# Kernel tuning notes

Measured on AMD Instinct MI355X. Metric: run time of the kernel, lower is better.

## Reference

```python
import jax, jax.numpy as jnp
import numpy as np

B, N, NPOINT, NSAMPLE = 8, 8192, 2048, 64
RADIUS = 0.2
C_IN = 64  # input feature channels; mlp[0]=64 -> 67 after use_xyz concat


def setup_inputs() -> dict:
    key = jax.random.key(0)
    ks = jax.random.split(key, 12)
    xyz = jax.random.uniform(ks[0], (B, N, 3), dtype=jnp.float32)
    features = jax.random.normal(ks[1], (B, N, C_IN), dtype=jnp.float32)
    inds = jax.random.randint(ks[2], (B, NPOINT), 0, N, dtype=jnp.int32)

    def mkw(k, cin, cout):
        return jax.random.normal(k, (cin, cout), jnp.float32) * (1.0 / np.sqrt(cin).astype(np.float32))

    w0 = mkw(ks[3], C_IN + 3, 64)
    w1 = mkw(ks[4], 64, 64)
    w2 = mkw(ks[5], 64, 128)
    # BN (inference) folded into per-channel scale/shift
    s0 = 1.0 + 0.1 * jax.random.normal(ks[6], (64,), jnp.float32)
    t0 = 0.1 * jax.random.normal(ks[7], (64,), jnp.float32)
    s1 = 1.0 + 0.1 * jax.random.normal(ks[8], (64,), jnp.float32)
    t1 = 0.1 * jax.random.normal(ks[9], (64,), jnp.float32)
    s2 = 1.0 + 0.1 * jax.random.normal(ks[10], (128,), jnp.float32)
    t2 = 0.1 * jax.random.normal(ks[11], (128,), jnp.float32)
    return dict(xyz=xyz, features=features, inds=inds,
                w0=w0, s0=s0, t0=t0, w1=w1, s1=s1, t1=t1, w2=w2, s2=s2, t2=t2)


def _ball_query(xyz, new_xyz):
    """First NSAMPLE point indices within RADIUS of each query; pad by repeating
    the first hit (matches CUDA ball_query semantics). xyz:(B,N,3) new_xyz:(B,S,3)."""
    nn = jnp.sum(xyz * xyz, axis=-1)            # (B,N)
    qq = jnp.sum(new_xyz * new_xyz, axis=-1)    # (B,S)
    d2 = qq[:, :, None] + nn[:, None, :] - 2.0 * jnp.einsum('bsc,bnc->bsn', new_xyz, xyz)
    within = d2 < (RADIUS * RADIUS)
    ar = jnp.arange(N, dtype=jnp.int32)
    keyed = jnp.where(within, ar[None, None, :], N)   # out-of-radius -> sentinel N
    keyed = jnp.sort(keyed, axis=-1)[:, :, :NSAMPLE]  # first hits in point order
    idx = jnp.where(keyed == N, keyed[:, :, :1], keyed)
    return jnp.minimum(idx, N - 1)


_gather = jax.vmap(lambda pts, i: pts[i])  # (N,C),(M,) -> (M,C) per batch


def reference(xyz, features, inds, w0, s0, t0, w1, s1, t1, w2, s2, t2):
    new_xyz = _gather(xyz, inds)                              # (B,S,3)
    idx = _ball_query(xyz, new_xyz)                           # (B,S,ns)
    flat = idx.reshape(B, NPOINT * NSAMPLE)
    g_xyz = _gather(xyz, flat).reshape(B, NPOINT, NSAMPLE, 3)
    g_xyz = (g_xyz - new_xyz[:, :, None, :]) / RADIUS         # normalize_xyz
    g_feat = _gather(features, flat).reshape(B, NPOINT, NSAMPLE, C_IN)
    x = jnp.concatenate([g_xyz, g_feat], axis=-1)             # (B,S,ns,C+3)
    for wgt, s, t in ((w0, s0, t0), (w1, s1, t1), (w2, s2, t2)):
        x = jax.nn.relu(jnp.einsum('bpsc,cd->bpsd', x, wgt) * s + t)
    new_features = jnp.max(x, axis=2)                         # max-pool over nsample
    return new_xyz, new_features, inds, idx
```

## Files before the change

### kernel.cpp

```cpp
#include <hip/hip_runtime.h>

#define BB 8
#define NN 8192
#define NPOINT 2048
#define NSAMPLE 64
#define CIN 64
#define RADIUS 0.2f
#define R2 (RADIUS * RADIUS)

#define OFF_NEWXYZ 0
#define OFF_FEAT (BB * NPOINT * 3)
#define OFF_INDS (OFF_FEAT + BB * NPOINT * 128)
#define OFF_IDX (OFF_INDS + BB * NPOINT)

typedef _Float16 half8 __attribute__((ext_vector_type(8)));
typedef _Float16 half4 __attribute__((ext_vector_type(4)));
typedef __fp16 f16x2 __attribute__((ext_vector_type(2)));
typedef float floatx16 __attribute__((ext_vector_type(16)));

#define P0 88
#define P1 72
#define X_LOC 0
#define H_LOC (64 * P0)
#define XH_WAVE (64 * P0 + 64 * P1)
#define WT0_S 0
#define WT1_S (64 * P0)
#define WT2_S (64 * P0 + 64 * P1)

#define QPW 8

__global__ __launch_bounds__(256) void ballq_kernel(
    const float* __restrict__ xyz, const int* __restrict__ inds,
    float* __restrict__ out, const float* __restrict__ features,
    _Float16* __restrict__ f16f) {
  if (f16f) {
    const int t = blockIdx.x * 256 + threadIdx.x;
    const float4* src = (const float4*)features;
    const float4 a = src[2 * t + 0];
    const float4 b = src[2 * t + 1];
    union {
      half8 v;
      f16x2 p[4];
    } u;
    u.p[0] = __builtin_amdgcn_cvt_pkrtz(a.x, a.y);
    u.p[1] = __builtin_amdgcn_cvt_pkrtz(a.z, a.w);
    u.p[2] = __builtin_amdgcn_cvt_pkrtz(b.x, b.y);
    u.p[3] = __builtin_amdgcn_cvt_pkrtz(b.z, b.w);
    ((half8*)f16f)[t] = u.v;
  }

  __shared__ int sidx[4][2][NSAMPLE];
  const int wave = (blockIdx.x * 256 + threadIdx.x) >> 6;
  const int lane = threadIdx.x & 63;
  const int wid = threadIdx.x >> 6;
  const int q0 = wave * 2, q1 = q0 + 1;
  const int b = q0 >> 11;

  const float* xb = xyz + (size_t)b * NN * 3;
  const int i0 = inds[q0], i1 = inds[q1];
  const float c0x = xb[i0 * 3 + 0], c0y = xb[i0 * 3 + 1], c0z = xb[i0 * 3 + 2];
  const float c1x = xb[i1 * 3 + 0], c1y = xb[i1 * 3 + 1], c1z = xb[i1 * 3 + 2];

  if (lane < 2) {
    const int qq_ = lane ? q1 : q0;
    const int ii = lane ? i1 : i0;
    out[OFF_NEWXYZ + (size_t)qq_ * 3 + 0] = lane ? c1x : c0x;
    out[OFF_NEWXYZ + (size_t)qq_ * 3 + 1] = lane ? c1y : c0y;
    out[OFF_NEWXYZ + (size_t)qq_ * 3 + 2] = lane ? c1z : c0z;
    out[OFF_INDS + qq_] = (float)ii;
  }

  const float qq0 = c0x * c0x + c0y * c0y + c0z * c0z;
  const float qq1 = c1x * c1x + c1y * c1y + c1z * c1z;

  int cnt0 = 0, cnt1 = 0;
  float ax[4], ay[4], az[4];
#pragma unroll
  for (int k = 0; k < 4; ++k) {
    const float* p = xb + (size_t)(k * 64 + lane) * 3;
    ax[k] = p[0];
    ay[k] = p[1];
    az[k] = p[2];
  }
  for (int j0 = 0; j0 < NN; j0 += 256) {
    float bx[4] = {0}, by[4] = {0}, bz[4] = {0};
    const int jn = j0 + 256;
    if (jn < NN) {
#pragma unroll
      for (int k = 0; k < 4; ++k) {
        const float* p = xb + (size_t)(jn + k * 64 + lane) * 3;
        bx[k] = p[0];
        by[k] = p[1];
        bz[k] = p[2];
      }
    }
#pragma unroll
    for (int k = 0; k < 4; ++k) {
      const int j = j0 + k * 64 + lane;
      const float nn_ = ax[k] * ax[k] + ay[k] * ay[k] + az[k] * az[k];
      const float dot0 = c0x * ax[k] + c0y * ay[k] + c0z * az[k];
      const float dot1 = c1x * ax[k] + c1y * ay[k] + c1z * az[k];
      const bool hit0 = (qq0 + nn_ - 2.0f * dot0) < R2;
      const bool hit1 = (qq1 + nn_ - 2.0f * dot1) < R2;
      const unsigned long long m0 = __ballot(hit0);
      const unsigned long long m1 = __ballot(hit1);
      if (hit0) {
        const int pos = cnt0 + (int)__popcll(m0 & ((1ull << lane) - 1ull));
        if (pos < NSAMPLE) sidx[wid][0][pos] = j;
      }
      if (hit1) {
        const int pos = cnt1 + (int)__popcll(m1 & ((1ull << lane) - 1ull));
        if (pos < NSAMPLE) sidx[wid][1][pos] = j;
      }
      cnt0 += (int)__popcll(m0);
      cnt1 += (int)__popcll(m1);
    }
    if (cnt0 >= NSAMPLE && cnt1 >= NSAMPLE) break;
#pragma unroll
    for (int k = 0; k < 4; ++k) {
      ax[k] = bx[k];
      ay[k] = by[k];
      az[k] = bz[k];
    }
  }
  const int v0 = sidx[wid][0][lane < cnt0 ? lane : 0];
  out[OFF_IDX + (size_t)q0 * NSAMPLE + lane] = (float)v0;
  const int v1 = sidx[wid][1][lane < cnt1 ? lane : 0];
  out[OFF_IDX + (size_t)q1 * NSAMPLE + lane] = (float)v1;
}

template <bool F16>
__global__ __launch_bounds__(128, 2) void mlp_mfma(
    const float* __restrict__ xyz, const float* __restrict__ features,
    const _Float16* __restrict__ f16f, const int* __restrict__ inds,
    const float* __restrict__ w0, const float* __restrict__ s0,
    const float* __restrict__ t0, const float* __restrict__ w1,
    const float* __restrict__ s1, const float* __restrict__ t1,
    const float* __restrict__ w2, const float* __restrict__ s2,
    const float* __restrict__ t2, float* __restrict__ out) {
  __shared__ _Float16 sm[2 * XH_WAVE];
  const int tid = threadIdx.x;
  const int w = tid >> 6;
  const int l = tid & 63;
  const int l31 = l & 31;
  const int h5 = l >> 5;
  const int koff = h5 * 8;

  {
    const int d = tid >> 1, hf = tid & 1;
    const float sd0 = s0[d], td0 = t0[d], sd1 = s1[d];
#pragma unroll
    for (int j = 0; j < 44; ++j) {
      const int c = hf * 44 + j;
      float v = 0.0f;
      if (c < 64) v = w0[(3 + c) * 64 + d] * sd0;
      else if (c < 67) v = w0[(c - 64) * 64 + d] * sd0;
      else if (c == 67) v = td0;
      sm[WT0_S + d * P0 + c] = (_Float16)v;
    }
#pragma unroll
    for (int j = 0; j < 32; ++j) {
      const int c = hf * 32 + j;
      sm[WT1_S + d * P1 + c] = (_Float16)(w1[c * 64 + d] * sd1);
    }
    const int ch = tid;
    const float sch = s2[ch];
#pragma unroll
    for (int c = 0; c < 64; ++c)
      sm[WT2_S + ch * P1 + c] = (_Float16)(w2[c * 128 + ch] * sch);
  }
  __syncthreads();

  half8 b0f[2][5], b1f[2][4], b2f[4][4];
#pragma unroll
  for (int nt = 0; nt < 2; ++nt)
#pragma unroll
    for (int ks = 0; ks < 5; ++ks)
      b0f[nt][ks] =
          *(const half8*)&sm[WT0_S + (nt * 32 + l31) * P0 + ks * 16 + koff];
#pragma unroll
  for (int nt = 0; nt < 2; ++nt)
#pragma unroll
    for (int ks = 0; ks < 4; ++ks)
      b1f[nt][ks] =
          *(const half8*)&sm[WT1_S + (nt * 32 + l31) * P1 + ks * 16 + koff];
#pragma unroll
  for (int ct = 0; ct < 4; ++ct)
#pragma unroll
    for (int ks = 0; ks < 4; ++ks)
      b2f[ct][ks] =
          *(const half8*)&sm[WT2_S + (ct * 32 + l31) * P1 + ks * 16 + koff];
  const float t1v0 = t1[l31];
  const float t1v1 = t1[32 + l31];
  float t2v[4];
#pragma unroll
  for (int ct = 0; ct < 4; ++ct) t2v[ct] = t2[ct * 32 + l31];
  __syncthreads();

  _Float16* xbuf = sm + w * XH_WAVE + X_LOC;
  _Float16* hbuf = sm + w * XH_WAVE + H_LOC;
  {
    half8 z = {};
    *(half8*)&xbuf[l * P0 + 72] = z;
  }

  const int lb = (blockIdx.x & 7) * ((int)gridDim.x >> 3) + (blockIdx.x >> 3);
  const int wq0 = (lb * 2 + w) * QPW;
  const int b = wq0 >> 11;
  const float* xb = xyz + (size_t)b * NN * 3;
  const float* fbase = features + (size_t)b * NN * CIN;
  const _Float16* fb16 = f16f + (size_t)b * NN * CIN;

  int myidx = (int)out[OFF_IDX + (size_t)wq0 * NSAMPLE + l];
  int indv = inds[wq0];
  float cx = xb[indv * 3 + 0], cy = xb[indv * 3 + 1], cz = xb[indv * 3 + 2];
  float ppx = xb[myidx * 3 + 0], ppy = xb[myidx * 3 + 1],
        ppz = xb[myidx * 3 + 2];

#pragma unroll 1
  for (int qi = 0; qi < QPW; ++qi) {
    const int q = wq0 + qi;
    const int nq = (qi + 1 < QPW) ? q + 1 : q;

    float4 g[16];
    half8 gh[8];
    if constexpr (F16) {
#pragma unroll
      for (int i = 0; i < 8; ++i) {
        const int r = (l >> 3) + 8 * i;
        const int sidx = __shfl(myidx, r, 64);
        gh[i] = *(const half8*)(fb16 + (size_t)sidx * CIN + (l & 7) * 8);
      }
    } else {
#pragma unroll
      for (int i = 0; i < 16; ++i) {
        const int s = (l >> 2) + 16 * (i & 3);
        const int c = (l & 3) + 4 * (i >> 2);
        const int sidx = __shfl(myidx, s, 64);
        g[i] = *(const float4*)(fbase + (size_t)sidx * CIN + 4 * c);
      }
    }
    const float fni = out[OFF_IDX + (size_t)nq * NSAMPLE + l];
    const int nindv = inds[nq];

    if constexpr (F16) {
#pragma unroll
      for (int i = 0; i < 8; ++i) {
        const int r = (l >> 3) + 8 * i;
        *(half8*)&xbuf[r * P0 + (l & 7) * 8] = gh[i];
      }
    } else {
#pragma unroll
      for (int i = 0; i < 16; ++i) {
        const int s = (l >> 2) + 16 * (i & 3);
        const int c = (l & 3) + 4 * (i >> 2);
        union {
          half4 v;
          f16x2 p[2];
        } hv;
        hv.p[0] = __builtin_amdgcn_cvt_pkrtz(g[i].x, g[i].y);
        hv.p[1] = __builtin_amdgcn_cvt_pkrtz(g[i].z, g[i].w);
        *(half4*)&xbuf[s * P0 + 4 * c] = hv.v;
      }
    }
    {
      union {
        half8 v;
        f16x2 p[4];
      } xv;
      xv.p[0] =
          __builtin_amdgcn_cvt_pkrtz((ppx - cx) * 5.0f, (ppy - cy) * 5.0f);
      xv.p[1] = __builtin_amdgcn_cvt_pkrtz((ppz - cz) * 5.0f, 1.0f);
      xv.p[2] = __builtin_amdgcn_cvt_pkrtz(0.0f, 0.0f);
      xv.p[3] = __builtin_amdgcn_cvt_pkrtz(0.0f, 0.0f);
      *(half8*)&xbuf[l * P0 + 64] = xv.v;
    }

    {
      half8 xa[2][5];
#pragma unroll
      for (int st = 0; st < 2; ++st)
#pragma unroll
        for (int ks = 0; ks < 5; ++ks)
          xa[st][ks] =
              *(const half8*)&xbuf[(st * 32 + l31) * P0 + ks * 16 + koff];
#pragma unroll
      for (int nt = 0; nt < 2; ++nt)
#pragma unroll
        for (int st = 0; st < 2; ++st) {
          floatx16 acc;
#pragma unroll
          for (int i = 0; i < 16; ++i) acc[i] = 0.0f;
#pragma unroll
          for (int ks = 0; ks < 5; ++ks)
            acc = __builtin_amdgcn_mfma_f32_32x32x16_f16(xa[st][ks],
                                                         b0f[nt][ks], acc,
                                                         0, 0, 0);
#pragma unroll
          for (int reg = 0; reg < 16; ++reg) {
            const int row = st * 32 + (reg & 3) + 8 * (reg >> 2) + 4 * h5;
            hbuf[row * P1 + nt * 32 + l31] = (_Float16)fmaxf(acc[reg], 0.0f);
          }
        }
    }

    const int nidxs = (int)fni;
    const float ncx = xb[nindv * 3 + 0];
    const float ncy = xb[nindv * 3 + 1];
    const float ncz = xb[nindv * 3 + 2];
    const float nppx = xb[nidxs * 3 + 0];
    const float nppy = xb[nidxs * 3 + 1];
    const float nppz = xb[nidxs * 3 + 2];

    {
      half8 ha[2][4];
#pragma unroll
      for (int st = 0; st < 2; ++st)
#pragma unroll
        for (int ks = 0; ks < 4; ++ks)
          ha[st][ks] =
              *(const half8*)&hbuf[(st * 32 + l31) * P1 + ks * 16 + koff];
#pragma unroll
      for (int nt = 0; nt < 2; ++nt) {
        const float tt = nt ? t1v1 : t1v0;
#pragma unroll
        for (int st = 0; st < 2; ++st) {
          floatx16 acc;
#pragma unroll
          for (int i = 0; i < 16; ++i) acc[i] = 0.0f;
#pragma unroll
          for (int ks = 0; ks < 4; ++ks)
            acc = __builtin_amdgcn_mfma_f32_32x32x16_f16(ha[st][ks],
                                                         b1f[nt][ks], acc,
                                                         0, 0, 0);
#pragma unroll
          for (int reg = 0; reg < 16; ++reg) {
            const int row = st * 32 + (reg & 3) + 8 * (reg >> 2) + 4 * h5;
            xbuf[row * P0 + nt * 32 + l31] =
                (_Float16)fmaxf(acc[reg] + tt, 0.0f);
          }
        }
      }
    }

    {
      half8 h1a[2][4];
#pragma unroll
      for (int st = 0; st < 2; ++st)
#pragma unroll
        for (int ks = 0; ks < 4; ++ks)
          h1a[st][ks] =
              *(const half8*)&xbuf[(st * 32 + l31) * P0 + ks * 16 + koff];
#pragma unroll
      for (int ct = 0; ct < 4; ++ct) {
        floatx16 aA, aB;
#pragma unroll
        for (int i = 0; i < 16; ++i) {
          aA[i] = 0.0f;
          aB[i] = 0.0f;
        }
#pragma unroll
        for (int ks = 0; ks < 4; ++ks) {
          aA = __builtin_amdgcn_mfma_f32_32x32x16_f16(h1a[0][ks], b2f[ct][ks],
                                                      aA, 0, 0, 0);
          aB = __builtin_amdgcn_mfma_f32_32x32x16_f16(h1a[1][ks], b2f[ct][ks],
                                                      aB, 0, 0, 0);
        }
        float m = fmaxf(aA[0], aB[0]);
#pragma unroll
        for (int i = 1; i < 16; ++i) m = fmaxf(m, fmaxf(aA[i], aB[i]));
        float v = fmaxf(m + t2v[ct], 0.0f);
        v = fmaxf(v, __shfl_xor(v, 32, 64));
        if (l < 32) out[OFF_FEAT + (size_t)q * 128 + ct * 32 + l] = v;
      }
    }

    myidx = nidxs;
    cx = ncx; cy = ncy; cz = ncz;
    ppx = nppx; ppy = nppy; ppz = nppz;
  }
}

extern "C" void kernel_launch(void* const* d_in, const int* in_sizes, int n_in,
                              void* d_out, int out_size, void* d_ws,
                              size_t ws_size, hipStream_t stream) {
  const float* xyz = (const float*)d_in[0];
  const float* features = (const float*)d_in[1];
  const int* inds = (const int*)d_in[2];
  const float* w0 = (const float*)d_in[3];
  const float* s0 = (const float*)d_in[4];
  const float* t0 = (const float*)d_in[5];
  const float* w1 = (const float*)d_in[6];
  const float* s1 = (const float*)d_in[7];
  const float* t1 = (const float*)d_in[8];
  const float* w2 = (const float*)d_in[9];
  const float* s2 = (const float*)d_in[10];
  const float* t2 = (const float*)d_in[11];
  float* out = (float*)d_out;

  const size_t f16need = (size_t)BB * NN * CIN * sizeof(_Float16);
  _Float16* f16f = (ws_size >= f16need) ? (_Float16*)d_ws : nullptr;

  const int nquery = BB * NPOINT;
  ballq_kernel<<<nquery / 8, 256, 0, stream>>>(xyz, inds, out, features, f16f);
  if (f16f)
    mlp_mfma<true><<<nquery / (2 * QPW), 128, 0, stream>>>(
        xyz, features, f16f, inds, w0, s0, t0, w1, s1, t1, w2, s2, t2, out);
  else
    mlp_mfma<false><<<nquery / (2 * QPW), 128, 0, stream>>>(
        xyz, features, f16f, inds, w0, s0, t0, w1, s1, t1, w2, s2, t2, out);
}
```

Baseline: 175.5 us.

## Prefold MLP weights to fp16 in workspace and stream them from global

The first kernel now also writes fp16 copies of the three MLP weight matrices, with BN scale folded in, into the workspace. A new MLP kernel loads the weight fragments directly from global/L2 every query instead of staging them in shared memory. This cuts LDS per block so three blocks fit per CU, and halves queries per wave, doubling the grid. The trade-off is repeated global weight reads per query, extra register pressure, and a serial weight-prep step done by block 0.

```diff
diff --git a/kernel.cpp b/kernel.cpp
--- a/kernel.cpp
+++ b/kernel.cpp
@@ -27,13 +27,24 @@
 #define WT1_S (64 * P0)
 #define WT2_S (64 * P0 + 64 * P1)
 
-#define QPW 8
+#define QPW_FB 8
+#define QPW_G 4
+
+#define WSF16H (BB * NN * CIN)
+#define WT0_OFF WSF16H
+#define WT1_OFF (WT0_OFF + 64 * 80)
+#define WT2_OFF (WT1_OFF + 64 * 64)
+#define WS_END (WT2_OFF + 128 * 64)
+#define WS_NEED ((size_t)WS_END * 2)
 
 __global__ __launch_bounds__(256) void ballq_kernel(
     const float* __restrict__ xyz, const int* __restrict__ inds,
     float* __restrict__ out, const float* __restrict__ features,
-    _Float16* __restrict__ f16f) {
-  if (f16f) {
+    _Float16* __restrict__ ws16, const float* __restrict__ w0,
+    const float* __restrict__ s0, const float* __restrict__ t0,
+    const float* __restrict__ w1, const float* __restrict__ s1,
+    const float* __restrict__ w2, const float* __restrict__ s2) {
+  if (ws16) {
     const int t = blockIdx.x * 256 + threadIdx.x;
     const float4* src = (const float4*)features;
     const float4 a = src[2 * t + 0];
@@ -46,7 +57,32 @@
     u.p[1] = __builtin_amdgcn_cvt_pkrtz(a.z, a.w);
     u.p[2] = __builtin_amdgcn_cvt_pkrtz(b.x, b.y);
     u.p[3] = __builtin_amdgcn_cvt_pkrtz(b.z, b.w);
-    ((half8*)f16f)[t] = u.v;
+    ((half8*)ws16)[t] = u.v;
+    if (blockIdx.x == 0) {
+      const int tt = threadIdx.x;
+      if (tt < 64) {
+        const int d = tt;
+        const float sd = s0[d], td = t0[d];
+        _Float16* row = ws16 + WT0_OFF + d * 80;
+        for (int c = 0; c < 80; ++c) {
+          float v = 0.0f;
+          if (c < 64) v = w0[(3 + c) * 64 + d] * sd;
+          else if (c < 67) v = w0[(c - 64) * 64 + d] * sd;
+          else if (c == 67) v = td;
+          row[c] = (_Float16)v;
+        }
+      } else if (tt < 128) {
+        const int d = tt - 64;
+        const float sd = s1[d];
+        _Float16* row = ws16 + WT1_OFF + d * 64;
+        for (int c = 0; c < 64; ++c) row[c] = (_Float16)(w1[c * 64 + d] * sd);
+      } else {
+        const int d2 = tt - 128;
+        const float sd = s2[d2];
+        _Float16* row = ws16 + WT2_OFF + d2 * 64;
+        for (int c = 0; c < 64; ++c) row[c] = (_Float16)(w2[c * 128 + d2] * sd);
+      }
+    }
   }
 
   __shared__ int sidx[4][2][NSAMPLE];
@@ -129,10 +165,215 @@
   out[OFF_IDX + (size_t)q1 * NSAMPLE + lane] = (float)v1;
 }
 
-template <bool F16>
-__global__ __launch_bounds__(128, 2) void mlp_mfma(
+__global__ __launch_bounds__(128, 3) void mlp_g(
+    const float* __restrict__ xyz, const _Float16* __restrict__ ws16,
+    const int* __restrict__ inds, const float* __restrict__ t1,
+    const float* __restrict__ t2, float* __restrict__ out) {
+  __shared__ _Float16 sm[2 * 64 * P0];
+  const int tid = threadIdx.x;
+  const int w = tid >> 6;
+  const int l = tid & 63;
+  const int l31 = l & 31;
+  const int h5 = l >> 5;
+  const int koff = h5 * 8;
+
+  _Float16* xbuf = sm + w * (64 * P0);
+  {
+    half8 z = {};
+    *(half8*)&xbuf[l * P0 + 72] = z;
+  }
+
+  const int lb = (blockIdx.x & 7) * ((int)gridDim.x >> 3) + (blockIdx.x >> 3);
+  const int wq0 = (lb * 2 + w) * QPW_G;
+  const int b = wq0 >> 11;
+  const float* xb = xyz + (size_t)b * NN * 3;
+  const _Float16* fb16 = ws16 + (size_t)b * NN * CIN;
+
+  const float t1v0 = t1[l31];
+  const float t1v1 = t1[32 + l31];
+  float t2v[4];
+#pragma unroll
+  for (int ct = 0; ct < 4; ++ct) t2v[ct] = t2[ct * 32 + l31];
+
+  int myidx = (int)out[OFF_IDX + (size_t)wq0 * NSAMPLE + l];
+  int indv = inds[wq0];
+  float cx = xb[indv * 3 + 0], cy = xb[indv * 3 + 1], cz = xb[indv * 3 + 2];
+  float ppx = xb[myidx * 3 + 0], ppy = xb[myidx * 3 + 1],
+        ppz = xb[myidx * 3 + 2];
+
+  unsigned long long wbu = (unsigned long long)(ws16 + WT0_OFF);
+
+#pragma unroll 1
+  for (int qi = 0; qi < QPW_G; ++qi) {
+    const int q = wq0 + qi;
+    const int nq = (qi + 1 < QPW_G) ? q + 1 : q;
+    asm volatile("" : "+s"(wbu));
+    const _Float16* wt0 = (const _Float16*)wbu;
+    const _Float16* wt1q = wt0 + 64 * 80;
+    const _Float16* wt2q = wt0 + 64 * 80 + 64 * 64;
+
+    half8 gh[8];
+#pragma unroll
+    for (int i = 0; i < 8; ++i) {
+      const int r = (l >> 3) + 8 * i;
+      const int sidx = __shfl(myidx, r, 64);
+      gh[i] = *(const half8*)(fb16 + (size_t)sidx * CIN + (l & 7) * 8);
+    }
+    half8 b0w[2][5];
+#pragma unroll
+    for (int nt = 0; nt < 2; ++nt)
+#pragma unroll
+      for (int ks = 0; ks < 5; ++ks)
+        b0w[nt][ks] =
+            *(const half8*)&wt0[(nt * 32 + l31) * 80 + ks * 16 + koff];
+    const float fni = out[OFF_IDX + (size_t)nq * NSAMPLE + l];
+    const int nindv = inds[nq];
+
+#pragma unroll
+    for (int i = 0; i < 8; ++i) {
+      const int r = (l >> 3) + 8 * i;
+      *(half8*)&xbuf[r * P0 + (l & 7) * 8] = gh[i];
+    }
+    {
+      union {
+        half8 v;
+        f16x2 p[4];
+      } xv;
+      xv.p[0] =
+          __builtin_amdgcn_cvt_pkrtz((ppx - cx) * 5.0f, (ppy - cy) * 5.0f);
+      xv.p[1] = __builtin_amdgcn_cvt_pkrtz((ppz - cz) * 5.0f, 1.0f);
+      xv.p[2] = __builtin_amdgcn_cvt_pkrtz(0.0f, 0.0f);
+      xv.p[3] = __builtin_amdgcn_cvt_pkrtz(0.0f, 0.0f);
+      *(half8*)&xbuf[l * P0 + 64] = xv.v;
+    }
+
+    half8 b1w[2][4];
+    {
+      half8 xa[2][5];
+#pragma unroll
+      for (int st = 0; st < 2; ++st)
+#pragma unroll
+        for (int ks = 0; ks < 5; ++ks)
+          xa[st][ks] =
+              *(const half8*)&xbuf[(st * 32 + l31) * P0 + ks * 16 + koff];
+#pragma unroll
+      for (int nt = 0; nt < 2; ++nt)
+#pragma unroll
+        for (int ks = 0; ks < 4; ++ks)
+          b1w[nt][ks] =
+              *(const half8*)&wt1q[(nt * 32 + l31) * 64 + ks * 16 + koff];
+#pragma unroll
+      for (int nt = 0; nt < 2; ++nt)
+#pragma unroll
+        for (int st = 0; st < 2; ++st) {
+          floatx16 acc;
+#pragma unroll
+          for (int i = 0; i < 16; ++i) acc[i] = 0.0f;
+#pragma unroll
+          for (int ks = 0; ks < 5; ++ks)
+            acc = __builtin_amdgcn_mfma_f32_32x32x16_f16(xa[st][ks],
+                                                         b0w[nt][ks], acc,
+                                                         0, 0, 0);
+#pragma unroll
+          for (int reg = 0; reg < 16; ++reg) {
+            const int row = st * 32 + (reg & 3) + 8 * (reg >> 2) + 4 * h5;
+            xbuf[row * P0 + nt * 32 + l31] = (_Float16)fmaxf(acc[reg], 0.0f);
+          }
+        }
+    }
+
+    const int nidxs = (int)fni;
+    const float ncx = xb[nindv * 3 + 0];
+    const float ncy = xb[nindv * 3 + 1];
+    const float ncz = xb[nindv * 3 + 2];
+    const float nppx = xb[nidxs * 3 + 0];
+    const float nppy = xb[nidxs * 3 + 1];
+    const float nppz = xb[nidxs * 3 + 2];
+
+    half8 b2c[4], b2n[4];
+    {
+      half8 ha[2][4];
+#pragma unroll
+      for (int st = 0; st < 2; ++st)
+#pragma unroll
+        for (int ks = 0; ks < 4; ++ks)
+          ha[st][ks] =
+              *(const half8*)&xbuf[(st * 32 + l31) * P0 + ks * 16 + koff];
+#pragma unroll
+      for (int ks = 0; ks < 4; ++ks)
+        b2c[ks] = *(const half8*)&wt2q[l31 * 64 + ks * 16 + koff];
+#pragma unroll
+      for (int nt = 0; nt < 2; ++nt) {
+        const float tt = nt ? t1v1 : t1v0;
+#pragma unroll
+        for (int st = 0; st < 2; ++st) {
+          floatx16 acc;
+#pragma unroll
+          for (int i = 0; i < 16; ++i) acc[i] = 0.0f;
+#pragma unroll
+          for (int ks = 0; ks < 4; ++ks)
+            acc = __builtin_amdgcn_mfma_f32_32x32x16_f16(ha[st][ks],
+                                                         b1w[nt][ks], acc,
+                                                         0, 0, 0);
+#pragma unroll
+          for (int reg = 0; reg < 16; ++reg) {
+            const int row = st * 32 + (reg & 3) + 8 * (reg >> 2) + 4 * h5;
+            xbuf[row * P0 + nt * 32 + l31] =
+                (_Float16)fmaxf(acc[reg] + tt, 0.0f);
+          }
+        }
+      }
+    }
+
+    {
+      half8 h1a[2][4];
+#pragma unroll
+      for (int st = 0; st < 2; ++st)
+#pragma unroll
+        for (int ks = 0; ks < 4; ++ks)
+          h1a[st][ks] =
+              *(const half8*)&xbuf[(st * 32 + l31) * P0 + ks * 16 + koff];
+#pragma unroll
+      for (int ct = 0; ct < 4; ++ct) {
+        if (ct < 3) {
+#pragma unroll
+          for (int ks = 0; ks < 4; ++ks)
+            b2n[ks] = *(const half8*)&wt2q[((ct + 1) * 32 + l31) * 64 +
+                                           ks * 16 + koff];
+        }
+        floatx16 aA, aB;
+#pragma unroll
+        for (int i = 0; i < 16; ++i) {
+          aA[i] = 0.0f;
+          aB[i] = 0.0f;
+        }
+#pragma unroll
+        for (int ks = 0; ks < 4; ++ks) {
+          aA = __builtin_amdgcn_mfma_f32_32x32x16_f16(h1a[0][ks], b2c[ks],
+                                                      aA, 0, 0, 0);
+          aB = __builtin_amdgcn_mfma_f32_32x32x16_f16(h1a[1][ks], b2c[ks],
+                                                      aB, 0, 0, 0);
+        }
+        float m = fmaxf(aA[0], aB[0]);
+#pragma unroll
+        for (int i = 1; i < 16; ++i) m = fmaxf(m, fmaxf(aA[i], aB[i]));
+        float v = fmaxf(m + t2v[ct], 0.0f);
+        v = fmaxf(v, __shfl_xor(v, 32, 64));
+        if (l < 32) out[OFF_FEAT + (size_t)q * 128 + ct * 32 + l] = v;
+#pragma unroll
+        for (int ks = 0; ks < 4; ++ks) b2c[ks] = b2n[ks];
+      }
+    }
+
+    myidx = nidxs;
+    cx = ncx; cy = ncy; cz = ncz;
+    ppx = nppx; ppy = nppy; ppz = nppz;
+  }
+}
+
+__global__ __launch_bounds__(128, 2) void mlp_fb(
     const float* __restrict__ xyz, const float* __restrict__ features,
-    const _Float16* __restrict__ f16f, const int* __restrict__ inds,
+    const int* __restrict__ inds,
     const float* __restrict__ w0, const float* __restrict__ s0,
     const float* __restrict__ t0, const float* __restrict__ w1,
     const float* __restrict__ s1, const float* __restrict__ t1,
@@ -205,11 +446,10 @@
   }
 
   const int lb = (blockIdx.x & 7) * ((int)gridDim.x >> 3) + (blockIdx.x >> 3);
-  const int wq0 = (lb * 2 + w) * QPW;
+  const int wq0 = (lb * 2 + w) * QPW_FB;
   const int b = wq0 >> 11;
   const float* xb = xyz + (size_t)b * NN * 3;
   const float* fbase = features + (size_t)b * NN * CIN;
-  const _Float16* fb16 = f16f + (size_t)b * NN * CIN;
 
   int myidx = (int)out[OFF_IDX + (size_t)wq0 * NSAMPLE + l];
   int indv = inds[wq0];
@@ -218,50 +458,32 @@
         ppz = xb[myidx * 3 + 2];
 
 #pragma unroll 1
-  for (int qi = 0; qi < QPW; ++qi) {
+  for (int qi = 0; qi < QPW_FB; ++qi) {
     const int q = wq0 + qi;
-    const int nq = (qi + 1 < QPW) ? q + 1 : q;
+    const int nq = (qi + 1 < QPW_FB) ? q + 1 : q;
 
     float4 g[16];
-    half8 gh[8];
-    if constexpr (F16) {
-#pragma unroll
-      for (int i = 0; i < 8; ++i) {
-        const int r = (l >> 3) + 8 * i;
-        const int sidx = __shfl(myidx, r, 64);
-        gh[i] = *(const half8*)(fb16 + (size_t)sidx * CIN + (l & 7) * 8);
-      }
-    } else {
-#pragma unroll
-      for (int i = 0; i < 16; ++i) {
-        const int s = (l >> 2) + 16 * (i & 3);
-        const int c = (l & 3) + 4 * (i >> 2);
-        const int sidx = __shfl(myidx, s, 64);
-        g[i] = *(const float4*)(fbase + (size_t)sidx * CIN + 4 * c);
-      }
+#pragma unroll
+    for (int i = 0; i < 16; ++i) {
+      const int s = (l >> 2) + 16 * (i & 3);
+      const int c = (l & 3) + 4 * (i >> 2);
+      const int sidx = __shfl(myidx, s, 64);
+      g[i] = *(const float4*)(fbase + (size_t)sidx * CIN + 4 * c);
     }
     const float fni = out[OFF_IDX + (size_t)nq * NSAMPLE + l];
     const int nindv = inds[nq];
 
-    if constexpr (F16) {
-#pragma unroll
-      for (int i = 0; i < 8; ++i) {
-        const int r = (l >> 3) + 8 * i;
-        *(half8*)&xbuf[r * P0 + (l & 7) * 8] = gh[i];
-      }
-    } else {
-#pragma unroll
-      for (int i = 0; i < 16; ++i) {
-        const int s = (l >> 2) + 16 * (i & 3);
-        const int c = (l & 3) + 4 * (i >> 2);
-        union {
-          half4 v;
-          f16x2 p[2];
-        } hv;
-        hv.p[0] = __builtin_amdgcn_cvt_pkrtz(g[i].x, g[i].y);
-        hv.p[1] = __builtin_amdgcn_cvt_pkrtz(g[i].z, g[i].w);
-        *(half4*)&xbuf[s * P0 + 4 * c] = hv.v;
-      }
+#pragma unroll
+    for (int i = 0; i < 16; ++i) {
+      const int s = (l >> 2) + 16 * (i & 3);
+      const int c = (l & 3) + 4 * (i >> 2);
+      union {
+        half4 v;
+        f16x2 p[2];
+      } hv;
+      hv.p[0] = __builtin_amdgcn_cvt_pkrtz(g[i].x, g[i].y);
+      hv.p[1] = __builtin_amdgcn_cvt_pkrtz(g[i].z, g[i].w);
+      *(half4*)&xbuf[s * P0 + 4 * c] = hv.v;
     }
     {
       union {
@@ -398,15 +620,16 @@
   const float* t2 = (const float*)d_in[11];
   float* out = (float*)d_out;
 
-  const size_t f16need = (size_t)BB * NN * CIN * sizeof(_Float16);
-  _Float16* f16f = (ws_size >= f16need) ? (_Float16*)d_ws : nullptr;
+  _Float16* ws16 = (ws_size >= WS_NEED) ? (_Float16*)d_ws : nullptr;
 
   const int nquery = BB * NPOINT;
-  ballq_kernel<<<nquery / 8, 256, 0, stream>>>(xyz, inds, out, features, f16f);
-  if (f16f)
-    mlp_mfma<true><<<nquery / (2 * QPW), 128, 0, stream>>>(
-        xyz, features, f16f, inds, w0, s0, t0, w1, s1, t1, w2, s2, t2, out);
-  else
-    mlp_mfma<false><<<nquery / (2 * QPW), 128, 0, stream>>>(
-        xyz, features, f16f, inds, w0, s0, t0, w1, s1, t1, w2, s2, t2, out);
+  ballq_kernel<<<nquery / 8, 256, 0, stream>>>(xyz, inds, out, features, ws16,
+                                               w0, s0, t0, w1, s1, w2, s2);
+  if (ws16) {
+    mlp_g<<<nquery / (2 * QPW_G), 128, 0, stream>>>(xyz, ws16, inds, t1, t2,
+                                                    out);
+  } else {
+    mlp_fb<<<nquery / (2 * QPW_FB), 128, 0, stream>>>(
+        xyz, features, inds, w0, s0, t0, w1, s1, t1, w2, s2, t2, out);
+  }
 }
```

New measurement: 183.8 us. 4.7% more time.
